# Optimization experiments

Measured on AMD Instinct MI355X. Metric: run time of the kernel, lower is better.

## Reference

```python
import jax, jax.numpy as jnp
import numpy as np

N_NODES = 50000
N_EDGES = 800000
N_INC = 64
E_OUTC = 64
HS1 = 128
HS2 = 128
LN_EPS = 1e-5


def setup_inputs() -> dict:
    key = jax.random.key(0)
    ks = jax.random.split(key, 8)
    scale1 = 1.0 / np.sqrt(N_INC + E_OUTC)
    scale2 = 1.0 / np.sqrt(HS1)
    return {
        "x": jax.random.normal(ks[0], (N_NODES, N_INC), dtype=jnp.float32),
        "edge_attr": jax.random.normal(ks[1], (N_EDGES, E_OUTC), dtype=jnp.float32),
        "edge_index": jax.random.randint(ks[2], (2, N_EDGES), 0, N_NODES, dtype=jnp.int64)
        if jax.config.jax_enable_x64 else jax.random.randint(ks[2], (2, N_EDGES), 0, N_NODES, dtype=jnp.int32),
        "W1": jax.random.normal(ks[3], (N_INC + E_OUTC, HS1), dtype=jnp.float32) * scale1,
        "b1": jnp.zeros((HS1,), dtype=jnp.float32),
        "ln_g": jnp.ones((HS1,), dtype=jnp.float32),
        "ln_b": jnp.zeros((HS1,), dtype=jnp.float32),
        "W2": jax.random.normal(ks[4], (HS1, HS2), dtype=jnp.float32) * scale2,
        "b2": jnp.zeros((HS2,), dtype=jnp.float32),
    }


def reference(x, edge_attr, edge_index, W1, b1, ln_g, ln_b, W2, b2):
    # _agg: gather source nodes, concat with edge features -> [E, n_inc+e_outc]
    row, col = edge_index[0], edge_index[1]
    h = jnp.concatenate([x[row], edge_attr], axis=1)
    # node_mlp_1: Linear -> LayerNorm -> ReLU -> Linear
    h = h @ W1 + b1
    mu = jnp.mean(h, axis=-1, keepdims=True)
    var = jnp.mean(jnp.square(h - mu), axis=-1, keepdims=True)
    h = (h - mu) * jax.lax.rsqrt(var + LN_EPS) * ln_g + ln_b
    h = jax.nn.relu(h)
    h = h @ W2 + b2  # [E, HS2]
    # scatter_mean into destination nodes, dim_size = N
    n = x.shape[0]
    sums = jax.ops.segment_sum(h, col, num_segments=n)
    cnt = jax.ops.segment_sum(jnp.ones((h.shape[0],), dtype=h.dtype), col, num_segments=n)
    return sums / jnp.maximum(cnt, 1.0)[:, None]
```

## Files before the change

### kernel.cpp

```cpp
#include <hip/hip_runtime.h>
#include <hip/hip_bf16.h>


typedef __bf16 bf16x8 __attribute__((ext_vector_type(8)));
typedef float f32x4 __attribute__((ext_vector_type(4)));

#define LN_EPS 1e-5f

__device__ __forceinline__ unsigned short bfbits(float f) {
  return __builtin_bit_cast(unsigned short, (__bf16)f);
}
__device__ __forceinline__ float bflo(unsigned int u) { return __uint_as_float(u << 16); }
__device__ __forceinline__ float bfhi(unsigned int u) { return __uint_as_float(u & 0xffff0000u); }
__device__ __forceinline__ unsigned int pkbf(float a, float b) {
  return (unsigned int)bfbits(a) | ((unsigned int)bfbits(b) << 16);
}

__global__ void hist_kernel(const int* __restrict__ eidx, int* __restrict__ cnt, int E) {
  int e = blockIdx.x * blockDim.x + threadIdx.x;
  if (e < E) atomicAdd(&cnt[eidx[E + e]], 1);
}

__global__ void scan_kernel(const int* __restrict__ cnt, int* __restrict__ off, int n) {
  __shared__ int wsum[16];
  __shared__ int carry_s;
  const int tid = threadIdx.x;
  const int wv = tid >> 6;
  const int ln = tid & 63;
  if (tid == 0) carry_s = 0;
  __syncthreads();
  for (int base = 0; base < n; base += 4096) {
    int i0 = base + tid * 4;
    int a = (i0 < n) ? cnt[i0] : 0;
    int b = (i0 + 1 < n) ? cnt[i0 + 1] : 0;
    int c = (i0 + 2 < n) ? cnt[i0 + 2] : 0;
    int d = (i0 + 3 < n) ? cnt[i0 + 3] : 0;
    int lsum = a + b + c + d;
    int sc = lsum;
#pragma unroll
    for (int dl = 1; dl < 64; dl <<= 1) {
      int t = __shfl_up(sc, dl);
      if (ln >= dl) sc += t;
    }
    if (ln == 63) wsum[wv] = sc;
    __syncthreads();
    int woff = 0;
#pragma unroll
    for (int w = 0; w < 16; ++w) {
      int t = wsum[w];
      if (w < wv) woff += t;
    }
    int excl = carry_s + woff + sc - lsum;
    if (i0 < n) off[i0] = excl;
    if (i0 + 1 < n) off[i0 + 1] = excl + a;
    if (i0 + 2 < n) off[i0 + 2] = excl + a + b;
    if (i0 + 3 < n) off[i0 + 3] = excl + a + b + c;
    __syncthreads();
    if (tid == 1023) carry_s = carry_s + woff + sc;
    __syncthreads();
  }
}

__global__ void scatter_kernel(const int* __restrict__ eidx, const int* __restrict__ off,
                               int* __restrict__ cur, int* __restrict__ perm, int E) {
  int e = blockIdx.x * blockDim.x + threadIdx.x;
  if (e < E) {
    int c = eidx[E + e];
    int p = atomicAdd(&cur[c], 1);
    perm[off[c] + p] = e;
  }
}

template <bool ATOMIC>
__global__ __launch_bounds__(1024, 1) void mlp_kernel(
    const float* __restrict__ x, const float* __restrict__ ea,
    const int* __restrict__ eidx, const int* __restrict__ perm,
    const int* __restrict__ cnt, const float* __restrict__ W1,
    const float* __restrict__ b1, const float* __restrict__ lng,
    const float* __restrict__ lnb, const float* __restrict__ W2,
    const float* __restrict__ b2, float* __restrict__ out, int E, int ntiles) {
  __shared__ __align__(16) unsigned int w1L[2048 * 4];
  __shared__ __align__(16) unsigned int w2L[2048 * 4];
  __shared__ float b1L[128];
  __shared__ float b2L[128];
  __shared__ unsigned int glcL[128];
  __shared__ __align__(16) char hbuf[16][16 * 272];

  const int tid = threadIdx.x;
  const int lane = tid & 63;
  const int wv = tid >> 6;
  const int e15 = lane & 15;
  const int q = lane >> 4;
  char* hb = hbuf[wv];

  for (int c = tid; c < 2048; c += 1024) {
    const int fragid = c >> 6;
    const int l = c & 63;
    const int ks = fragid >> 3, mt = fragid & 7;
    const int qq = l >> 4, ee = l & 15;
    const size_t base = (size_t)(ks * 32 + qq * 8) * 128 + mt * 16 + ee;
    unsigned int p1[4], p2[4];
#pragma unroll
    for (int jj = 0; jj < 4; ++jj) {
      p1[jj] = pkbf(W1[base + (size_t)(2 * jj) * 128], W1[base + (size_t)(2 * jj + 1) * 128]);
      p2[jj] = pkbf(W2[base + (size_t)(2 * jj) * 128], W2[base + (size_t)(2 * jj + 1) * 128]);
    }
    uint4 v1 = {p1[0], p1[1], p1[2], p1[3]};
    uint4 v2 = {p2[0], p2[1], p2[2], p2[3]};
    *(uint4*)&w1L[c * 4] = v1;
    *(uint4*)&w2L[c * 4] = v2;
  }
  if (tid < 128) {
    b1L[tid] = b1[tid];
    b2L[tid] = b2[tid];
    glcL[tid] = pkbf(lng[tid], lnb[tid]);
  }
  __syncthreads();

  const int nwav = (gridDim.x * blockDim.x) >> 6;
  const int wid = (blockIdx.x * blockDim.x + tid) >> 6;

  auto mlp_core = [&](const float4 (&raw)[8], f32x4 (&c2)[8]) {
    bf16x8 bfr[4];
#pragma unroll
    for (int ks = 0; ks < 4; ++ks) {
      const float* p0 = (const float*)&raw[2 * ks];
      const float* p1 = (const float*)&raw[2 * ks + 1];
#pragma unroll
      for (int j = 0; j < 4; ++j) {
        bfr[ks][j] = (__bf16)p0[j];
        bfr[ks][4 + j] = (__bf16)p1[j];
      }
    }
    f32x4 c1[8];
#pragma unroll
    for (int mt = 0; mt < 8; ++mt) {
      float4 bv = *(const float4*)&b1L[mt * 16 + q * 4];
      c1[mt][0] = bv.x;
      c1[mt][1] = bv.y;
      c1[mt][2] = bv.z;
      c1[mt][3] = bv.w;
    }
#pragma unroll
    for (int ks = 0; ks < 4; ++ks)
#pragma unroll
      for (int mt = 0; mt < 8; ++mt) {
        bf16x8 wf = __builtin_bit_cast(
            bf16x8, *(const uint4*)&w1L[((ks * 8 + mt) * 64 + lane) * 4]);
        c1[mt] = __builtin_amdgcn_mfma_f32_16x16x32_bf16(wf, bfr[ks], c1[mt], 0, 0, 0);
      }

    float s = 0.f, ss = 0.f;
#pragma unroll
    for (int mt = 0; mt < 8; ++mt)
#pragma unroll
      for (int r = 0; r < 4; ++r) {
        float v = c1[mt][r];
        s += v;
        ss += v * v;
      }
    s += __shfl_xor(s, 16);
    s += __shfl_xor(s, 32);
    ss += __shfl_xor(ss, 16);
    ss += __shfl_xor(ss, 32);
    const float mu = s * 0.0078125f;
    const float var = ss * 0.0078125f - mu * mu;
    const float inv = rsqrtf(var + LN_EPS);
#pragma unroll
    for (int mt = 0; mt < 8; ++mt) {
      uint4 gv = *(const uint4*)&glcL[mt * 16 + q * 4];
      unsigned int g[4] = {gv.x, gv.y, gv.z, gv.w};
      unsigned short u[4];
#pragma unroll
      for (int r = 0; r < 4; ++r) {
        float v = (c1[mt][r] - mu) * inv;
        v = v * bflo(g[r]) + bfhi(g[r]);
        v = fmaxf(v, 0.f);
        u[r] = bfbits(v);
      }
      uint2 w;
      w.x = (unsigned int)u[0] | ((unsigned int)u[1] << 16);
      w.y = (unsigned int)u[2] | ((unsigned int)u[3] << 16);
      *(uint2*)(hb + e15 * 272 + mt * 32 + q * 8) = w;
    }
    bf16x8 hf[4];
#pragma unroll
    for (int ks = 0; ks < 4; ++ks)
      hf[ks] = __builtin_bit_cast(bf16x8, *(const uint4*)(hb + e15 * 272 + ks * 64 + q * 16));
#pragma unroll
    for (int mt = 0; mt < 8; ++mt) {
      float4 bv = *(const float4*)&b2L[mt * 16 + q * 4];
      c2[mt][0] = bv.x;
      c2[mt][1] = bv.y;
      c2[mt][2] = bv.z;
      c2[mt][3] = bv.w;
    }
#pragma unroll
    for (int ks = 0; ks < 4; ++ks)
#pragma unroll
      for (int mt = 0; mt < 8; ++mt) {
        bf16x8 wf = __builtin_bit_cast(
            bf16x8, *(const uint4*)&w2L[((ks * 8 + mt) * 64 + lane) * 4]);
        c2[mt] = __builtin_amdgcn_mfma_f32_16x16x32_bf16(wf, hf[ks], c2[mt], 0, 0, 0);
      }
  };

  auto reduce_store = [&](const f32x4 (&c2)[8], int nd, float inv) {
#pragma unroll
    for (int mt = 0; mt < 8; ++mt) {
      unsigned short u[4];
#pragma unroll
      for (int r = 0; r < 4; ++r) u[r] = bfbits(c2[mt][r]);
      uint2 w;
      w.x = (unsigned int)u[0] | ((unsigned int)u[1] << 16);
      w.y = (unsigned int)u[2] | ((unsigned int)u[3] << 16);
      *(uint2*)(hb + e15 * 272 + mt * 32 + q * 8) = w;
    }
    float acc0 = 0.f, acc1 = 0.f;
    int curn = __shfl(nd, 0);
    float cinv = __shfl(inv, 0);
#pragma unroll
    for (int i = 0; i < 16; ++i) {
      int ni = __shfl(nd, i);
      float ii = __shfl(inv, i);
      if (ni != curn) {
        unsafeAtomicAdd(out + (size_t)curn * 128 + lane * 2, acc0 * cinv);
        unsafeAtomicAdd(out + (size_t)curn * 128 + lane * 2 + 1, acc1 * cinv);
        acc0 = 0.f;
        acc1 = 0.f;
        curn = ni;
        cinv = ii;
      }
      unsigned int v = *(const unsigned int*)(hb + i * 272 + lane * 4);
      acc0 += bflo(v);
      acc1 += bfhi(v);
    }
    unsafeAtomicAdd(out + (size_t)curn * 128 + lane * 2, acc0 * cinv);
    unsafeAtomicAdd(out + (size_t)curn * 128 + lane * 2 + 1, acc1 * cinv);
  };

#define LOADRAW(dst, rowv, ev)                              \
  do {                                                      \
    const float* xr_ = x + (size_t)(rowv)*64;               \
    const float* ar_ = ea + (size_t)(ev)*64;                \
    dst[0] = *(const float4*)(xr_ + q * 8);                 \
    dst[1] = *(const float4*)(xr_ + q * 8 + 4);             \
    dst[2] = *(const float4*)(xr_ + 32 + q * 8);            \
    dst[3] = *(const float4*)(xr_ + 32 + q * 8 + 4);        \
    dst[4] = *(const float4*)(ar_ + q * 8);                 \
    dst[5] = *(const float4*)(ar_ + q * 8 + 4);             \
    dst[6] = *(const float4*)(ar_ + 32 + q * 8);            \
    dst[7] = *(const float4*)(ar_ + 32 + q * 8 + 4);        \
  } while (0)

  if constexpr (!ATOMIC) {
    int tA = wid;
    if (tA >= ntiles) return;
    int pA = tA * 16 + e15;
    int eA = perm[pA];
    int rowA = eidx[eA];
    int ndA = eidx[E + eA];
    float invA = 1.f / (float)cnt[ndA];
    int tB = tA + nwav;
    int tBc = (tB < ntiles) ? tB : tA;
    int pB = tBc * 16 + e15;
    int eB = perm[pB];
    int rowB = eidx[eB];
    int ndB = eidx[E + eB];
    float invB = 1.f / (float)cnt[ndB];
    float4 rawA[8], rawB[8];
    LOADRAW(rawA, rowA, eA);

    for (int tb = tA; tb < ntiles; tb += 2 * nwav) {
      {
        int tn = tb + 2 * nwav;
        int tc = (tn < ntiles) ? tn : tb;
        int pn = tc * 16 + e15;
        int eAn = perm[pn];
        int rAn = eidx[eAn];
        int nAn = eidx[E + eAn];
        float iAn = 1.f / (float)cnt[nAn];
        LOADRAW(rawB, rowB, eB);
        f32x4 c2[8];
        mlp_core(rawA, c2);
        reduce_store(c2, ndA, invA);
        eA = eAn;
        rowA = rAn;
        ndA = nAn;
        invA = iAn;
      }
      {
        int tcur = tb + nwav;
        int tn = tb + 3 * nwav;
        int tc = (tn < ntiles) ? tn : tb;
        int pn = tc * 16 + e15;
        int eBn = perm[pn];
        int rBn = eidx[eBn];
        int nBn = eidx[E + eBn];
        float iBn = 1.f / (float)cnt[nBn];
        LOADRAW(rawA, rowA, eA);
        if (tcur < ntiles) {
          f32x4 c2[8];
          mlp_core(rawB, c2);
          reduce_store(c2, ndB, invB);
        }
        eB = eBn;
        rowB = rBn;
        ndB = nBn;
        invB = iBn;
      }
    }
  } else {
    for (int t = wid; t < ntiles; t += nwav) {
      const int pos = t * 16 + e15;
      const int e = pos;
      const int row = eidx[e];
      const int cl = eidx[E + e];
      float4 raw[8];
      LOADRAW(raw, row, e);
      f32x4 c2[8];
      mlp_core(raw, c2);
      float* op = out + (size_t)cl * 128 + q * 4;
#pragma unroll
      for (int mt = 0; mt < 8; ++mt)
#pragma unroll
        for (int r = 0; r < 4; ++r) unsafeAtomicAdd(op + mt * 16 + r, c2[mt][r]);
    }
  }
#undef LOADRAW
}

__global__ void divide_kernel(float* __restrict__ out, const int* __restrict__ cnt, int N) {
  int i = blockIdx.x * blockDim.x + threadIdx.x;
  if (i >= N * 32) return;
  int node = i >> 5;
  float s = 1.f / (float)(cnt[node] > 0 ? cnt[node] : 1);
  float4* p = (float4*)out + i;
  float4 v = *p;
  v.x *= s;
  v.y *= s;
  v.z *= s;
  v.w *= s;
  *p = v;
}

extern "C" void kernel_launch(void* const* d_in, const int* in_sizes, int n_in,
                              void* d_out, int out_size, void* d_ws, size_t ws_size,
                              hipStream_t stream) {
  const float* x = (const float*)d_in[0];
  const float* ea = (const float*)d_in[1];
  const int* eidx = (const int*)d_in[2];
  const float* W1 = (const float*)d_in[3];
  const float* b1 = (const float*)d_in[4];
  const float* lng = (const float*)d_in[5];
  const float* lnb = (const float*)d_in[6];
  const float* W2 = (const float*)d_in[7];
  const float* b2 = (const float*)d_in[8];
  float* out = (float*)d_out;

  const int N = in_sizes[0] / 64;
  const int E = in_sizes[1] / 64;
  const int ntiles = E / 16;
  const size_t permB = (size_t)E * 4;
  const size_t cB = (size_t)N * 4;
  const size_t need = permB + 3 * cB;
  const int eblocks = (E + 255) / 256;

  if (ws_size >= need) {
    int* perm = (int*)d_ws;
    int* cnt = perm + E;
    int* cur = cnt + N;
    int* off = cur + N;
    hipMemsetAsync(out, 0, (size_t)out_size * 4, stream);
    hipMemsetAsync(cnt, 0, 2 * cB, stream);
    hist_kernel<<<eblocks, 256, 0, stream>>>(eidx, cnt, E);
    scan_kernel<<<1, 1024, 0, stream>>>(cnt, off, N);
    scatter_kernel<<<eblocks, 256, 0, stream>>>(eidx, off, cur, perm, E);
    mlp_kernel<false><<<256, 1024, 0, stream>>>(x, ea, eidx, perm, cnt, W1, b1,
                                                lng, lnb, W2, b2, out, E, ntiles);
  } else {
    int* cnt = (int*)d_ws;
    hipMemsetAsync(out, 0, (size_t)out_size * 4, stream);
    hipMemsetAsync(cnt, 0, cB, stream);
    hist_kernel<<<eblocks, 256, 0, stream>>>(eidx, cnt, E);
    mlp_kernel<true><<<256, 1024, 0, stream>>>(x, ea, eidx, nullptr, cnt, W1, b1,
                                               lng, lnb, W2, b2, out, E, ntiles);
    divide_kernel<<<(N * 32 + 255) / 256, 256, 0, stream>>>(out, cnt, N);
  }
}
```

Before: 481.9 us.

## Process two edge tiles per wave per iteration sharing weight fragments

Each wave now handles a pair of adjacent 16-edge tiles together. Every W1/W2 LDS fragment load feeds two interleaved MFMA chains, which halves LDS weight traffic per edge and gives the MFMA pipeline independent work. In exchange it drops the previous software prefetch of raw inputs for the next tile, raises register pressure, and adds an even-tile-count requirement for the sorted path.

```diff
diff --git a/kernel.cpp b/kernel.cpp
--- a/kernel.cpp
+++ b/kernel.cpp
@@ -120,8 +120,18 @@
   const int nwav = (gridDim.x * blockDim.x) >> 6;
   const int wid = (blockIdx.x * blockDim.x + tid) >> 6;
 
-  auto mlp_core = [&](const float4 (&raw)[8], f32x4 (&c2)[8]) {
-    bf16x8 bfr[4];
+  auto load_cvt = [&](int rowv, int ev, bf16x8 (&bfr)[4]) {
+    const float* xr_ = x + (size_t)rowv * 64;
+    const float* ar_ = ea + (size_t)ev * 64;
+    float4 raw[8];
+    raw[0] = *(const float4*)(xr_ + q * 8);
+    raw[1] = *(const float4*)(xr_ + q * 8 + 4);
+    raw[2] = *(const float4*)(xr_ + 32 + q * 8);
+    raw[3] = *(const float4*)(xr_ + 32 + q * 8 + 4);
+    raw[4] = *(const float4*)(ar_ + q * 8);
+    raw[5] = *(const float4*)(ar_ + q * 8 + 4);
+    raw[6] = *(const float4*)(ar_ + 32 + q * 8);
+    raw[7] = *(const float4*)(ar_ + 32 + q * 8 + 4);
 #pragma unroll
     for (int ks = 0; ks < 4; ++ks) {
       const float* p0 = (const float*)&raw[2 * ks];
@@ -132,24 +142,9 @@
         bfr[ks][4 + j] = (__bf16)p1[j];
       }
     }
-    f32x4 c1[8];
-#pragma unroll
-    for (int mt = 0; mt < 8; ++mt) {
-      float4 bv = *(const float4*)&b1L[mt * 16 + q * 4];
-      c1[mt][0] = bv.x;
-      c1[mt][1] = bv.y;
-      c1[mt][2] = bv.z;
-      c1[mt][3] = bv.w;
-    }
-#pragma unroll
-    for (int ks = 0; ks < 4; ++ks)
-#pragma unroll
-      for (int mt = 0; mt < 8; ++mt) {
-        bf16x8 wf = __builtin_bit_cast(
-            bf16x8, *(const uint4*)&w1L[((ks * 8 + mt) * 64 + lane) * 4]);
-        c1[mt] = __builtin_amdgcn_mfma_f32_16x16x32_bf16(wf, bfr[ks], c1[mt], 0, 0, 0);
-      }
-
+  };
+
+  auto ln_stage_hf = [&](f32x4 (&c1)[8], bf16x8 (&hf)[4]) {
     float s = 0.f, ss = 0.f;
 #pragma unroll
     for (int mt = 0; mt < 8; ++mt)
@@ -183,26 +178,9 @@
       w.y = (unsigned int)u[2] | ((unsigned int)u[3] << 16);
       *(uint2*)(hb + e15 * 272 + mt * 32 + q * 8) = w;
     }
-    bf16x8 hf[4];
 #pragma unroll
     for (int ks = 0; ks < 4; ++ks)
       hf[ks] = __builtin_bit_cast(bf16x8, *(const uint4*)(hb + e15 * 272 + ks * 64 + q * 16));
-#pragma unroll
-    for (int mt = 0; mt < 8; ++mt) {
-      float4 bv = *(const float4*)&b2L[mt * 16 + q * 4];
-      c2[mt][0] = bv.x;
-      c2[mt][1] = bv.y;
-      c2[mt][2] = bv.z;
-      c2[mt][3] = bv.w;
-    }
-#pragma unroll
-    for (int ks = 0; ks < 4; ++ks)
-#pragma unroll
-      for (int mt = 0; mt < 8; ++mt) {
-        bf16x8 wf = __builtin_bit_cast(
-            bf16x8, *(const uint4*)&w2L[((ks * 8 + mt) * 64 + lane) * 4]);
-        c2[mt] = __builtin_amdgcn_mfma_f32_16x16x32_bf16(wf, hf[ks], c2[mt], 0, 0, 0);
-      }
   };
 
   auto reduce_store = [&](const f32x4 (&c2)[8], int nd, float inv) {
@@ -239,87 +217,114 @@
     unsafeAtomicAdd(out + (size_t)curn * 128 + lane * 2 + 1, acc1 * cinv);
   };
 
-#define LOADRAW(dst, rowv, ev)                              \
-  do {                                                      \
-    const float* xr_ = x + (size_t)(rowv)*64;               \
-    const float* ar_ = ea + (size_t)(ev)*64;                \
-    dst[0] = *(const float4*)(xr_ + q * 8);                 \
-    dst[1] = *(const float4*)(xr_ + q * 8 + 4);             \
-    dst[2] = *(const float4*)(xr_ + 32 + q * 8);            \
-    dst[3] = *(const float4*)(xr_ + 32 + q * 8 + 4);        \
-    dst[4] = *(const float4*)(ar_ + q * 8);                 \
-    dst[5] = *(const float4*)(ar_ + q * 8 + 4);             \
-    dst[6] = *(const float4*)(ar_ + 32 + q * 8);            \
-    dst[7] = *(const float4*)(ar_ + 32 + q * 8 + 4);        \
-  } while (0)
-
   if constexpr (!ATOMIC) {
-    int tA = wid;
-    if (tA >= ntiles) return;
-    int pA = tA * 16 + e15;
-    int eA = perm[pA];
-    int rowA = eidx[eA];
-    int ndA = eidx[E + eA];
+    const int nunits = ntiles >> 1;
+    int u = wid;
+    if (u >= nunits) return;
+    int pA = (2 * u) * 16 + e15;
+    int pB = (2 * u + 1) * 16 + e15;
+    int eA = perm[pA], eB = perm[pB];
+    int rowA = eidx[eA], rowB = eidx[eB];
+    int ndA = eidx[E + eA], ndB = eidx[E + eB];
     float invA = 1.f / (float)cnt[ndA];
-    int tB = tA + nwav;
-    int tBc = (tB < ntiles) ? tB : tA;
-    int pB = tBc * 16 + e15;
-    int eB = perm[pB];
-    int rowB = eidx[eB];
-    int ndB = eidx[E + eB];
     float invB = 1.f / (float)cnt[ndB];
-    float4 rawA[8], rawB[8];
-    LOADRAW(rawA, rowA, eA);
-
-    for (int tb = tA; tb < ntiles; tb += 2 * nwav) {
-      {
-        int tn = tb + 2 * nwav;
-        int tc = (tn < ntiles) ? tn : tb;
-        int pn = tc * 16 + e15;
-        int eAn = perm[pn];
-        int rAn = eidx[eAn];
-        int nAn = eidx[E + eAn];
-        float iAn = 1.f / (float)cnt[nAn];
-        LOADRAW(rawB, rowB, eB);
-        f32x4 c2[8];
-        mlp_core(rawA, c2);
-        reduce_store(c2, ndA, invA);
-        eA = eAn;
-        rowA = rAn;
-        ndA = nAn;
-        invA = iAn;
-      }
-      {
-        int tcur = tb + nwav;
-        int tn = tb + 3 * nwav;
-        int tc = (tn < ntiles) ? tn : tb;
-        int pn = tc * 16 + e15;
-        int eBn = perm[pn];
-        int rBn = eidx[eBn];
-        int nBn = eidx[E + eBn];
-        float iBn = 1.f / (float)cnt[nBn];
-        LOADRAW(rawA, rowA, eA);
-        if (tcur < ntiles) {
-          f32x4 c2[8];
-          mlp_core(rawB, c2);
-          reduce_store(c2, ndB, invB);
+
+    for (; u < nunits; u += nwav) {
+      int un = u + nwav;
+      int uc = (un < nunits) ? un : u;
+      int pAn = (2 * uc) * 16 + e15;
+      int pBn = (2 * uc + 1) * 16 + e15;
+      int eAn = perm[pAn], eBn = perm[pBn];
+      int rAn = eidx[eAn], rBn = eidx[eBn];
+      int nAn = eidx[E + eAn], nBn = eidx[E + eBn];
+      float iAn = 1.f / (float)cnt[nAn];
+      float iBn = 1.f / (float)cnt[nBn];
+
+      bf16x8 bfrA[4], bfrB[4];
+      load_cvt(rowA, eA, bfrA);
+      load_cvt(rowB, eB, bfrB);
+
+      f32x4 c1a[8], c1b[8];
+#pragma unroll
+      for (int mt = 0; mt < 8; ++mt) {
+        float4 bv = *(const float4*)&b1L[mt * 16 + q * 4];
+        c1a[mt][0] = bv.x; c1a[mt][1] = bv.y; c1a[mt][2] = bv.z; c1a[mt][3] = bv.w;
+        c1b[mt] = c1a[mt];
+      }
+#pragma unroll
+      for (int ks = 0; ks < 4; ++ks)
+#pragma unroll
+        for (int mt = 0; mt < 8; ++mt) {
+          bf16x8 wf = __builtin_bit_cast(
+              bf16x8, *(const uint4*)&w1L[((ks * 8 + mt) * 64 + lane) * 4]);
+          c1a[mt] = __builtin_amdgcn_mfma_f32_16x16x32_bf16(wf, bfrA[ks], c1a[mt], 0, 0, 0);
+          c1b[mt] = __builtin_amdgcn_mfma_f32_16x16x32_bf16(wf, bfrB[ks], c1b[mt], 0, 0, 0);
         }
-        eB = eBn;
-        rowB = rBn;
-        ndB = nBn;
-        invB = iBn;
-      }
+
+      bf16x8 hfA[4], hfB[4];
+      ln_stage_hf(c1a, hfA);
+      ln_stage_hf(c1b, hfB);
+
+      f32x4 c2a[8], c2b[8];
+#pragma unroll
+      for (int mt = 0; mt < 8; ++mt) {
+        float4 bv = *(const float4*)&b2L[mt * 16 + q * 4];
+        c2a[mt][0] = bv.x; c2a[mt][1] = bv.y; c2a[mt][2] = bv.z; c2a[mt][3] = bv.w;
+        c2b[mt] = c2a[mt];
+      }
+#pragma unroll
+      for (int ks = 0; ks < 4; ++ks)
+#pragma unroll
+        for (int mt = 0; mt < 8; ++mt) {
+          bf16x8 wf = __builtin_bit_cast(
+              bf16x8, *(const uint4*)&w2L[((ks * 8 + mt) * 64 + lane) * 4]);
+          c2a[mt] = __builtin_amdgcn_mfma_f32_16x16x32_bf16(wf, hfA[ks], c2a[mt], 0, 0, 0);
+          c2b[mt] = __builtin_amdgcn_mfma_f32_16x16x32_bf16(wf, hfB[ks], c2b[mt], 0, 0, 0);
+        }
+
+      reduce_store(c2a, ndA, invA);
+      reduce_store(c2b, ndB, invB);
+
+      eA = eAn; rowA = rAn; ndA = nAn; invA = iAn;
+      eB = eBn; rowB = rBn; ndB = nBn; invB = iBn;
     }
   } else {
     for (int t = wid; t < ntiles; t += nwav) {
-      const int pos = t * 16 + e15;
-      const int e = pos;
+      const int e = t * 16 + e15;
       const int row = eidx[e];
       const int cl = eidx[E + e];
-      float4 raw[8];
-      LOADRAW(raw, row, e);
+      bf16x8 bfr[4];
+      load_cvt(row, e, bfr);
+      f32x4 c1[8];
+#pragma unroll
+      for (int mt = 0; mt < 8; ++mt) {
+        float4 bv = *(const float4*)&b1L[mt * 16 + q * 4];
+        c1[mt][0] = bv.x; c1[mt][1] = bv.y; c1[mt][2] = bv.z; c1[mt][3] = bv.w;
+      }
+#pragma unroll
+      for (int ks = 0; ks < 4; ++ks)
+#pragma unroll
+        for (int mt = 0; mt < 8; ++mt) {
+          bf16x8 wf = __builtin_bit_cast(
+              bf16x8, *(const uint4*)&w1L[((ks * 8 + mt) * 64 + lane) * 4]);
+          c1[mt] = __builtin_amdgcn_mfma_f32_16x16x32_bf16(wf, bfr[ks], c1[mt], 0, 0, 0);
+        }
+      bf16x8 hf[4];
+      ln_stage_hf(c1, hf);
       f32x4 c2[8];
-      mlp_core(raw, c2);
+#pragma unroll
+      for (int mt = 0; mt < 8; ++mt) {
+        float4 bv = *(const float4*)&b2L[mt * 16 + q * 4];
+        c2[mt][0] = bv.x; c2[mt][1] = bv.y; c2[mt][2] = bv.z; c2[mt][3] = bv.w;
+      }
+#pragma unroll
+      for (int ks = 0; ks < 4; ++ks)
+#pragma unroll
+        for (int mt = 0; mt < 8; ++mt) {
+          bf16x8 wf = __builtin_bit_cast(
+              bf16x8, *(const uint4*)&w2L[((ks * 8 + mt) * 64 + lane) * 4]);
+          c2[mt] = __builtin_amdgcn_mfma_f32_16x16x32_bf16(wf, hf[ks], c2[mt], 0, 0, 0);
+        }
       float* op = out + (size_t)cl * 128 + q * 4;
 #pragma unroll
       for (int mt = 0; mt < 8; ++mt)
@@ -327,7 +332,6 @@
         for (int r = 0; r < 4; ++r) unsafeAtomicAdd(op + mt * 16 + r, c2[mt][r]);
     }
   }
-#undef LOADRAW
 }
 
 __global__ void divide_kernel(float* __restrict__ out, const int* __restrict__ cnt, int N) {
@@ -366,7 +370,7 @@
   const size_t need = permB + 3 * cB;
   const int eblocks = (E + 255) / 256;
 
-  if (ws_size >= need) {
+  if (ws_size >= need && (ntiles % 2) == 0) {
     int* perm = (int*)d_ws;
     int* cnt = perm + E;
     int* cur = cnt + N;
```

After: 584.2 us. 1.21x slower.

## Fuse histogram, scan and scatter into one persistent kernel with grid barriers

Applied to the files above, without the earlier changes.

Replaces the three preprocessing launches (atomic histogram, single-block scan, scatter into a destination-sorted permutation) with one persistent kernel sized to four blocks per CU. The stages are separated by software grid barriers built on agent-scope atomics. The scan becomes a two-level per-block plus block-offset scan instead of a serial single-block loop. This removes launch gaps and the single-block scan bottleneck, but relies on all blocks being co-resident for the spin barriers and adds barrier latency.

```diff
diff --git a/kernel.cpp b/kernel.cpp
--- a/kernel.cpp
+++ b/kernel.cpp
@@ -14,6 +14,91 @@
 __device__ __forceinline__ float bfhi(unsigned int u) { return __uint_as_float(u & 0xffff0000u); }
 __device__ __forceinline__ unsigned int pkbf(float a, float b) {
   return (unsigned int)bfbits(a) | ((unsigned int)bfbits(b) << 16);
+}
+
+__device__ __forceinline__ void gbar(int* slot) {
+  __syncthreads();
+  if (threadIdx.x == 0) {
+    __threadfence();
+    __hip_atomic_fetch_add(slot, 1, __ATOMIC_ACQ_REL, __HIP_MEMORY_SCOPE_AGENT);
+    while (__hip_atomic_load(slot, __ATOMIC_ACQUIRE, __HIP_MEMORY_SCOPE_AGENT) <
+           (int)gridDim.x)
+      __builtin_amdgcn_s_sleep(2);
+  }
+  __syncthreads();
+}
+
+__global__ __launch_bounds__(256, 4) void preproc_kernel(
+    const int* __restrict__ eidx, int* __restrict__ cnt, int* __restrict__ cur,
+    int* __restrict__ off, int* __restrict__ perm, int* __restrict__ blkSum,
+    int* __restrict__ blkOff, int* __restrict__ bar, int N, int E) {
+  __shared__ int ws[4];
+  const int tid = threadIdx.x;
+  const int nb = gridDim.x;
+  const int gtid = blockIdx.x * 256 + tid;
+  const int gsz = nb * 256;
+
+  for (int e = gtid; e < E; e += gsz) atomicAdd(&cnt[eidx[E + e]], 1);
+  gbar(&bar[0]);
+
+  const int CHUNK = (N + nb - 1) / nb;
+  const int base = blockIdx.x * CHUNK;
+  if (tid < 64) {
+    const int i = base + tid;
+    const int v = (tid < CHUNK && i < N) ? cnt[i] : 0;
+    int sc = v;
+#pragma unroll
+    for (int d = 1; d < 64; d <<= 1) {
+      int t = __shfl_up(sc, d);
+      if (tid >= d) sc += t;
+    }
+    if (tid < CHUNK && i < N) off[i] = sc - v;
+    if (tid == 63) blkSum[blockIdx.x] = sc;
+  }
+  gbar(&bar[1]);
+
+  if (blockIdx.x == 0) {
+    const int lane = tid & 63, wv = tid >> 6;
+    const int i0 = tid * 4;
+    int a = (i0 < nb) ? blkSum[i0] : 0;
+    int b = (i0 + 1 < nb) ? blkSum[i0 + 1] : 0;
+    int c = (i0 + 2 < nb) ? blkSum[i0 + 2] : 0;
+    int d = (i0 + 3 < nb) ? blkSum[i0 + 3] : 0;
+    int lsum = a + b + c + d;
+    int sc = lsum;
+#pragma unroll
+    for (int dl = 1; dl < 64; dl <<= 1) {
+      int t = __shfl_up(sc, dl);
+      if (lane >= dl) sc += t;
+    }
+    if (lane == 63) ws[wv] = sc;
+    __syncthreads();
+    int woff = 0;
+#pragma unroll
+    for (int w = 0; w < 4; ++w) {
+      int t = ws[w];
+      if (w < wv) woff += t;
+    }
+    const int excl = woff + sc - lsum;
+    if (i0 < nb) blkOff[i0] = excl;
+    if (i0 + 1 < nb) blkOff[i0 + 1] = excl + a;
+    if (i0 + 2 < nb) blkOff[i0 + 2] = excl + a + b;
+    if (i0 + 3 < nb) blkOff[i0 + 3] = excl + a + b + c;
+  }
+  gbar(&bar[2]);
+
+  {
+    const int boff = blkOff[blockIdx.x];
+    const int i = base + tid;
+    if (tid < CHUNK && i < N) off[i] += boff;
+  }
+  gbar(&bar[3]);
+
+  for (int e = gtid; e < E; e += gsz) {
+    int c = eidx[E + e];
+    int p = atomicAdd(&cur[c], 1);
+    perm[off[c] + p] = e;
+  }
 }
 
 __global__ void hist_kernel(const int* __restrict__ eidx, int* __restrict__ cnt, int E) {
@@ -361,21 +446,39 @@
   const int N = in_sizes[0] / 64;
   const int E = in_sizes[1] / 64;
   const int ntiles = E / 16;
-  const size_t permB = (size_t)E * 4;
   const size_t cB = (size_t)N * 4;
-  const size_t need = permB + 3 * cB;
+  const size_t need = ((size_t)E + 3 * (size_t)N + 8 + 2048) * 4;
   const int eblocks = (E + 255) / 256;
+
+  static int ncu = 0;
+  if (ncu == 0) {
+    int dev = 0;
+    hipGetDevice(&dev);
+    hipDeviceProp_t prop;
+    hipGetDeviceProperties(&prop, dev);
+    ncu = prop.multiProcessorCount;
+  }
+  int nbp = ncu * 4;
+  if (nbp > 1024) nbp = 1024;
 
   if (ws_size >= need) {
     int* perm = (int*)d_ws;
     int* cnt = perm + E;
     int* cur = cnt + N;
-    int* off = cur + N;
+    int* bar = cur + N;
+    int* off = bar + 8;
+    int* blkSum = off + N;
+    int* blkOff = blkSum + 1024;
     hipMemsetAsync(out, 0, (size_t)out_size * 4, stream);
-    hipMemsetAsync(cnt, 0, 2 * cB, stream);
-    hist_kernel<<<eblocks, 256, 0, stream>>>(eidx, cnt, E);
-    scan_kernel<<<1, 1024, 0, stream>>>(cnt, off, N);
-    scatter_kernel<<<eblocks, 256, 0, stream>>>(eidx, off, cur, perm, E);
+    hipMemsetAsync(cnt, 0, (2 * (size_t)N + 8) * 4, stream);
+    if (nbp > 0 && (size_t)nbp * 64 >= (size_t)N) {
+      preproc_kernel<<<nbp, 256, 0, stream>>>(eidx, cnt, cur, off, perm, blkSum,
+                                              blkOff, bar, N, E);
+    } else {
+      hist_kernel<<<eblocks, 256, 0, stream>>>(eidx, cnt, E);
+      scan_kernel<<<1, 1024, 0, stream>>>(cnt, off, N);
+      scatter_kernel<<<eblocks, 256, 0, stream>>>(eidx, off, cur, perm, E);
+    }
     mlp_kernel<false><<<256, 1024, 0, stream>>>(x, ea, eidx, perm, cnt, W1, b1,
                                                 lng, lnb, W2, b2, out, E, ntiles);
   } else {
```

After: 662.1 us. +37.4%, slower.
